# Optimization experiments

Measured on AMD Instinct MI355X. Metric: run time of the kernel, lower is better.

The kernel has to match this reference:

```python
import jax, jax.numpy as jnp
import numpy as np

B, S, D_ENC, D_DEC, UNITS = 64, 2048, 512, 512, 512


def setup_inputs() -> dict:
    key = jax.random.key(0)
    ks = jax.random.split(key, 8)
    enc = jax.random.normal(ks[0], (B, S, D_ENC), dtype=jnp.float32)
    dec = jax.random.normal(ks[1], (B, D_DEC), dtype=jnp.float32)
    # Dense params (glorot-ish scale)
    W1 = jax.random.normal(ks[2], (D_ENC, UNITS), dtype=jnp.float32) / np.sqrt(D_ENC)
    b1 = jnp.zeros((UNITS,), dtype=jnp.float32)
    W2 = jax.random.normal(ks[3], (D_DEC, UNITS), dtype=jnp.float32) / np.sqrt(D_DEC)
    b2 = jnp.zeros((UNITS,), dtype=jnp.float32)
    V = jax.random.normal(ks[4], (UNITS, 1), dtype=jnp.float32) / np.sqrt(UNITS)
    bv = jnp.zeros((1,), dtype=jnp.float32)
    return {"encoder_outputs": enc, "decoder_hidden": dec,
            "W1": W1, "b1": b1, "W2": W2, "b2": b2, "V": V, "bv": bv}


def reference(encoder_outputs, decoder_hidden, W1, b1, W2, b2, V, bv):
    # score_features: [B,S,U] = tanh(W1(enc) + W2(dec)[:,None,:])
    proj_enc = jnp.einsum('bsd,du->bsu', encoder_outputs, W1) + b1
    proj_dec = decoder_hidden @ W2 + b2                      # [B,U]
    feat = jnp.tanh(proj_enc + proj_dec[:, None, :])         # [B,S,U]
    score = jnp.einsum('bsu,uo->bso', feat, V) + bv          # [B,S,1]
    attn = jax.nn.softmax(score, axis=1)                     # softmax over seq
    context = jnp.sum(attn * encoder_outputs, axis=1)        # [B,D_enc]
    return context, jnp.squeeze(attn, axis=-1)
```

## Files before the change

### kernel.cpp

```cpp
#include <hip/hip_runtime.h>
#include <hip/hip_bf16.h>

#define BATCH 64
#define SEQ   2048
#define DIM   512
#define MROWS (BATCH * SEQ)

typedef short bf16x8 __attribute__((ext_vector_type(8)));
typedef float f32x4  __attribute__((ext_vector_type(4)));

static __device__ __forceinline__ unsigned short f2bf(float f) {
    union { float f; unsigned u; } v; v.f = f;
    unsigned u = v.u;
    u += 0x7FFFu + ((u >> 16) & 1u);
    return (unsigned short)(u >> 16);
}

static __device__ __forceinline__ float tanh_fast(float x) {
    float xc = fminf(20.0f, fmaxf(-20.0f, x));
#if __has_builtin(__builtin_amdgcn_exp2f)
    float t = __builtin_amdgcn_exp2f(2.885390082f * xc);
#else
    float t = exp2f(2.885390082f * xc);
#endif
#if __has_builtin(__builtin_amdgcn_rcpf)
    return (t - 1.0f) * __builtin_amdgcn_rcpf(t + 1.0f);
#else
    return (t - 1.0f) / (t + 1.0f);
#endif
}

typedef __attribute__((address_space(1))) const unsigned int gu32;
typedef __attribute__((address_space(3))) unsigned int lu32;
static __device__ __forceinline__ void gload_lds16(const unsigned short* g,
                                                   unsigned short* l) {
    __builtin_amdgcn_global_load_lds((gu32*)g, (lu32*)l, 16, 0, 0);
}

__global__ void prep_w1t_kernel(const float* __restrict__ W1,
                                unsigned short* __restrict__ w1t) {
    int stride = gridDim.x * blockDim.x;
    for (int i = blockIdx.x * blockDim.x + threadIdx.x; i < DIM * DIM; i += stride) {
        int k = i >> 9;
        int u = i & 511;
        w1t[u * DIM + k] = f2bf(W1[i]);
    }
}

__global__ void proj_dec_v2(const float* __restrict__ dec,
                            const float* __restrict__ W2,
                            const float* __restrict__ b1,
                            const float* __restrict__ b2,
                            float* __restrict__ pd) {
    __shared__ float sdec[DIM];
    __shared__ float red[4 * 64];
    const int ug = blockIdx.x;
    const int b  = blockIdx.y;
    const int t  = threadIdx.x;
    sdec[t]       = dec[b * DIM + t];
    sdec[t + 256] = dec[b * DIM + t + 256];
    __syncthreads();
    const int u  = ug * 64 + (t & 63);
    const int kq = t >> 6;
    float acc = 0.f;
    #pragma unroll 4
    for (int k = kq * 128; k < kq * 128 + 128; ++k)
        acc += sdec[k] * W2[k * DIM + u];
    red[kq * 64 + (t & 63)] = acc;
    __syncthreads();
    if (t < 64) {
        int u_g = ug * 64 + t;
        float s = red[t] + red[64 + t] + red[128 + t] + red[192 + t]
                + b1[u_g] + b2[u_g];
        pd[b * DIM + u_g] = s;
    }
}

#define BM3 64
#define BK3 64

__global__ __launch_bounds__(256, 2) void gemm_score_v4(
    const float* __restrict__ enc,
    const unsigned short* __restrict__ w1t,
    const float* __restrict__ pd,
    const float* __restrict__ V,
    float* __restrict__ scores)
{
    __shared__ unsigned short sA[BM3 * BK3];
    __shared__ unsigned short sB[DIM * BK3];

    const int tid  = threadIdx.x;
    const int lane = tid & 63;
    const int wave = tid >> 6;
    const int quad = lane >> 4;
    const int l15  = lane & 15;

    const int row0 = blockIdx.x * BM3;

    f32x4 acc[8][4];
    for (int j = 0; j < 8; ++j)
        for (int tr = 0; tr < 4; ++tr)
            acc[j][tr] = (f32x4){0.f, 0.f, 0.f, 0.f};

    for (int k0 = 0; k0 < DIM; k0 += BK3) {
        for (int i = 0; i < 16; ++i) {
            int c  = i * 256 + tid;
            int r  = c >> 3;
            int cc = c & 7;
            int gc = cc ^ (r & 7);
            gload_lds16(w1t + (size_t)r * DIM + k0 + gc * 8, &sB[c * 8]);
        }
        for (int i = 0; i < 2; ++i) {
            int c  = i * 256 + tid;
            int r  = c >> 3;
            int cc = c & 7;
            const float4* p =
                (const float4*)(enc + (size_t)(row0 + r) * DIM + k0 + cc * 8);
            float4 va = p[0], vb = p[1];
            union { ushort4 s[2]; uint4 q; } o;
            o.s[0].x = f2bf(va.x); o.s[0].y = f2bf(va.y);
            o.s[0].z = f2bf(va.z); o.s[0].w = f2bf(va.w);
            o.s[1].x = f2bf(vb.x); o.s[1].y = f2bf(vb.y);
            o.s[1].z = f2bf(vb.z); o.s[1].w = f2bf(vb.w);
            *(uint4*)(&sA[r * BK3 + ((cc ^ (r & 7)) * 8)]) = o.q;
        }
        __syncthreads();

        for (int kk = 0; kk < BK3; kk += 32) {
            int jc = (kk >> 3) + quad;
            bf16x8 af[4];
            for (int tr = 0; tr < 4; ++tr) {
                int am = tr * 16 + l15;
                af[tr] = *(const bf16x8*)(&sA[am * BK3 + ((jc ^ (am & 7)) * 8)]);
            }
            for (int j = 0; j < 8; ++j) {
                int u = wave * 128 + j * 16 + l15;
                bf16x8 bfr = *(const bf16x8*)(&sB[u * BK3 + ((jc ^ (u & 7)) * 8)]);
                for (int tr = 0; tr < 4; ++tr)
                    acc[j][tr] = __builtin_amdgcn_mfma_f32_16x16x32_bf16(
                        af[tr], bfr, acc[j][tr], 0, 0, 0);
            }
        }
        __syncthreads();
    }

    const int b = row0 >> 11;
    float sacc[4][4];
    for (int tr = 0; tr < 4; ++tr)
        for (int r = 0; r < 4; ++r) sacc[tr][r] = 0.f;

    for (int j = 0; j < 8; ++j) {
        int u_g   = wave * 128 + j * 16 + l15;
        float pdv = pd[b * DIM + u_g];
        float vv  = V[u_g];
        for (int tr = 0; tr < 4; ++tr)
            for (int r = 0; r < 4; ++r)
                sacc[tr][r] += tanh_fast(acc[j][tr][r] + pdv) * vv;
    }
    for (int tr = 0; tr < 4; ++tr)
        for (int r = 0; r < 4; ++r) {
            float v = sacc[tr][r];
            v += __shfl_xor(v, 1);
            v += __shfl_xor(v, 2);
            v += __shfl_xor(v, 4);
            v += __shfl_xor(v, 8);
            sacc[tr][r] = v;
        }
    float* red = (float*)sA;
    if (l15 == 0) {
        for (int tr = 0; tr < 4; ++tr)
            for (int r = 0; r < 4; ++r)
                red[wave * BM3 + tr * 16 + quad * 4 + r] = sacc[tr][r];
    }
    __syncthreads();
    if (tid < BM3) {
        float s = red[tid] + red[BM3 + tid] + red[2 * BM3 + tid] + red[3 * BM3 + tid];
        scores[row0 + tid] = s;
    }
}

__global__ __launch_bounds__(256) void softmax_context_kernel(
    const float* __restrict__ scores,
    const float* __restrict__ enc,
    float* __restrict__ attn,
    float* __restrict__ ctx) {
    __shared__ float sa[SEQ];
    __shared__ float red[32 * 64];
    const int dchunk = blockIdx.x;
    const int b      = blockIdx.y;
    const int t      = threadIdx.x;

    const float* sc = scores + (size_t)b * SEQ;
    float v[8];
    float mx = -1e30f;
    for (int i = 0; i < 8; ++i) {
        v[i] = sc[t + i * 256];
        mx = fmaxf(mx, v[i]);
    }
    red[t] = mx;
    __syncthreads();
    for (int off = 128; off > 0; off >>= 1) {
        if (t < off) red[t] = fmaxf(red[t], red[t + off]);
        __syncthreads();
    }
    mx = red[0];
    __syncthreads();
    float sum = 0.f;
    for (int i = 0; i < 8; ++i) {
        float e = expf(v[i] - mx);
        sa[t + i * 256] = e;
        sum += e;
    }
    red[t] = sum;
    __syncthreads();
    for (int off = 128; off > 0; off >>= 1) {
        if (t < off) red[t] += red[t + off];
        __syncthreads();
    }
    const float inv = 1.0f / red[0];
    __syncthreads();
    for (int i = 0; i < 8; ++i) sa[t + i * 256] *= inv;
    if (dchunk == 0) {
        for (int i = 0; i < 8; ++i)
            attn[(size_t)b * SEQ + t + i * 256] = sa[t + i * 256];
    }
    __syncthreads();

    const int tl = t & 7;
    const int rg = t >> 3;
    const float* base = enc + (size_t)b * SEQ * DIM + dchunk * 64 + tl * 8;
    float a[8];
    for (int q = 0; q < 8; ++q) a[q] = 0.f;
    for (int i = 0; i < 64; ++i) {
        int r = rg + i * 32;
        float w = sa[r];
        const float4* p = (const float4*)(base + (size_t)r * DIM);
        float4 x = p[0], y = p[1];
        a[0] += w * x.x; a[1] += w * x.y; a[2] += w * x.z; a[3] += w * x.w;
        a[4] += w * y.x; a[5] += w * y.y; a[6] += w * y.z; a[7] += w * y.w;
    }
    for (int q = 0; q < 8; ++q) red[rg * 64 + tl * 8 + q] = a[q];
    __syncthreads();
    if (t < 64) {
        float s = 0.f;
        for (int g = 0; g < 32; ++g) s += red[g * 64 + t];
        ctx[(size_t)b * DIM + dchunk * 64 + t] = s;
    }
}

extern "C" void kernel_launch(void* const* d_in, const int* in_sizes, int n_in,
                              void* d_out, int out_size, void* d_ws, size_t ws_size,
                              hipStream_t stream) {
    const float* enc = (const float*)d_in[0];
    const float* dec = (const float*)d_in[1];
    const float* W1  = (const float*)d_in[2];
    const float* b1  = (const float*)d_in[3];
    const float* W2  = (const float*)d_in[4];
    const float* b2  = (const float*)d_in[5];
    const float* V   = (const float*)d_in[6];

    float* out  = (float*)d_out;
    float* ctx  = out;
    float* attn = out + BATCH * DIM;

    char* ws = (char*)d_ws;
    float* pd            = (float*)ws;
    unsigned short* w1t  = (unsigned short*)(ws + 131072);
    float* scores        = (float*)(ws + 131072 + 524288);

    prep_w1t_kernel<<<256, 256, 0, stream>>>(W1, w1t);
    proj_dec_v2<<<dim3(8, BATCH), 256, 0, stream>>>(dec, W2, b1, b2, pd);
    gemm_score_v4<<<MROWS / BM3, 256, 0, stream>>>(enc, w1t, pd, V, scores);
    softmax_context_kernel<<<dim3(8, BATCH), 256, 0, stream>>>(scores, enc, attn, ctx);
}
```

Before: 468.1 us.

## Fuse softmax-weighted context accumulation into score GEMM with atomic partial sums

```diff
diff --git a/kernel.cpp b/kernel.cpp
--- a/kernel.cpp
+++ b/kernel.cpp
@@ -79,12 +79,14 @@
 #define BM3 64
 #define BK3 64
 
-__global__ __launch_bounds__(256, 2) void gemm_score_v4(
+__global__ __launch_bounds__(256, 2) void gemm_score_v6(
     const float* __restrict__ enc,
     const unsigned short* __restrict__ w1t,
     const float* __restrict__ pd,
     const float* __restrict__ V,
-    float* __restrict__ scores)
+    float* __restrict__ scores,
+    float* __restrict__ cnum,
+    float* __restrict__ zacc)
 {
     __shared__ unsigned short sA[BM3 * BK3];
     __shared__ unsigned short sB[DIM * BK3];
@@ -166,7 +168,8 @@
             v += __shfl_xor(v, 8);
             sacc[tr][r] = v;
         }
-    float* red = (float*)sA;
+    float* red  = (float*)sA;
+    float* eLds = ((float*)sA) + 256;
     if (l15 == 0) {
         for (int tr = 0; tr < 4; ++tr)
             for (int r = 0; r < 4; ++r)
@@ -176,75 +179,52 @@
     if (tid < BM3) {
         float s = red[tid] + red[BM3 + tid] + red[2 * BM3 + tid] + red[3 * BM3 + tid];
         scores[row0 + tid] = s;
-    }
-}
-
-__global__ __launch_bounds__(256) void softmax_context_kernel(
-    const float* __restrict__ scores,
-    const float* __restrict__ enc,
-    float* __restrict__ attn,
-    float* __restrict__ ctx) {
-    __shared__ float sa[SEQ];
-    __shared__ float red[32 * 64];
-    const int dchunk = blockIdx.x;
-    const int b      = blockIdx.y;
-    const int t      = threadIdx.x;
-
-    const float* sc = scores + (size_t)b * SEQ;
-    float v[8];
-    float mx = -1e30f;
-    for (int i = 0; i < 8; ++i) {
-        v[i] = sc[t + i * 256];
-        mx = fmaxf(mx, v[i]);
-    }
-    red[t] = mx;
-    __syncthreads();
-    for (int off = 128; off > 0; off >>= 1) {
-        if (t < off) red[t] = fmaxf(red[t], red[t + off]);
-        __syncthreads();
-    }
-    mx = red[0];
-    __syncthreads();
-    float sum = 0.f;
-    for (int i = 0; i < 8; ++i) {
-        float e = expf(v[i] - mx);
-        sa[t + i * 256] = e;
-        sum += e;
-    }
-    red[t] = sum;
-    __syncthreads();
-    for (int off = 128; off > 0; off >>= 1) {
-        if (t < off) red[t] += red[t + off];
-        __syncthreads();
-    }
-    const float inv = 1.0f / red[0];
-    __syncthreads();
-    for (int i = 0; i < 8; ++i) sa[t + i * 256] *= inv;
-    if (dchunk == 0) {
-        for (int i = 0; i < 8; ++i)
-            attn[(size_t)b * SEQ + t + i * 256] = sa[t + i * 256];
-    }
-    __syncthreads();
-
-    const int tl = t & 7;
-    const int rg = t >> 3;
-    const float* base = enc + (size_t)b * SEQ * DIM + dchunk * 64 + tl * 8;
-    float a[8];
-    for (int q = 0; q < 8; ++q) a[q] = 0.f;
-    for (int i = 0; i < 64; ++i) {
-        int r = rg + i * 32;
-        float w = sa[r];
-        const float4* p = (const float4*)(base + (size_t)r * DIM);
-        float4 x = p[0], y = p[1];
-        a[0] += w * x.x; a[1] += w * x.y; a[2] += w * x.z; a[3] += w * x.w;
-        a[4] += w * y.x; a[5] += w * y.y; a[6] += w * y.z; a[7] += w * y.w;
-    }
-    for (int q = 0; q < 8; ++q) red[rg * 64 + tl * 8 + q] = a[q];
-    __syncthreads();
-    if (t < 64) {
-        float s = 0.f;
-        for (int g = 0; g < 32; ++g) s += red[g * 64 + t];
-        ctx[(size_t)b * DIM + dchunk * 64 + t] = s;
+        eLds[tid] = expf(s);
+    }
+    __syncthreads();
+
+    if (wave == 0) {
+        float e = eLds[lane];
+        e += __shfl_xor(e, 32);
+        e += __shfl_xor(e, 16);
+        e += __shfl_xor(e, 8);
+        e += __shfl_xor(e, 4);
+        e += __shfl_xor(e, 2);
+        e += __shfl_xor(e, 1);
+        if (lane == 0) atomicAdd(&zacc[b], e);
+    }
+    {
+        const int d = tid * 2;
+        const float* ebase = enc + (size_t)row0 * DIM + d;
+        float cx = 0.f, cy = 0.f;
+        #pragma unroll 4
+        for (int r = 0; r < BM3; ++r) {
+            float w = eLds[r];
+            float2 x = *(const float2*)(ebase + (size_t)r * DIM);
+            cx += w * x.x;
+            cy += w * x.y;
+        }
+        atomicAdd(&cnum[b * DIM + d],     cx);
+        atomicAdd(&cnum[b * DIM + d + 1], cy);
+    }
+}
+
+__global__ void finalize_kernel(const float* __restrict__ scores,
+                                const float* __restrict__ cnum,
+                                const float* __restrict__ zacc,
+                                float* __restrict__ attn,
+                                float* __restrict__ ctx) {
+    const int c = blockIdx.x;
+    const int b = blockIdx.y;
+    const int t = threadIdx.x;
+    const float invZ = 1.0f / zacc[b];
+    for (int i = 0; i < 2; ++i) {
+        int s = c * 512 + t + i * 256;
+        attn[(size_t)b * SEQ + s] = expf(scores[(size_t)b * SEQ + s]) * invZ;
+    }
+    if (c == 0) {
+        ctx[b * DIM + t]       = cnum[b * DIM + t]       * invZ;
+        ctx[b * DIM + t + 256] = cnum[b * DIM + t + 256] * invZ;
     }
 }
 
@@ -267,9 +247,15 @@
     float* pd            = (float*)ws;
     unsigned short* w1t  = (unsigned short*)(ws + 131072);
     float* scores        = (float*)(ws + 131072 + 524288);
+    float* cnum          = (float*)(ws + 131072 + 524288 + 524288);
+    float* zacc          = (float*)(ws + 131072 + 524288 + 524288 + 131072);
+
+    hipMemsetAsync(cnum, 0, (size_t)BATCH * DIM * 4 + BATCH * 4, stream);
 
     prep_w1t_kernel<<<256, 256, 0, stream>>>(W1, w1t);
     proj_dec_v2<<<dim3(8, BATCH), 256, 0, stream>>>(dec, W2, b1, b2, pd);
-    gemm_score_v4<<<MROWS / BM3, 256, 0, stream>>>(enc, w1t, pd, V, scores);
-    softmax_context_kernel<<<dim3(8, BATCH), 256, 0, stream>>>(scores, enc, attn, ctx);
-}
+    gemm_score_v6<<<MROWS / BM3, 256, 0, stream>>>(enc, w1t, pd, V, scores,
+                                                   cnum, zacc);
+    finalize_kernel<<<dim3(4, BATCH), 256, 0, stream>>>(scores, cnum, zacc,
+                                                        attn, ctx);
+}
```

Result: faster. 448.1 us (-4.3%).
